# Optimization experiments

Hardware: AMD Instinct MI355X
Metric: run time of the kernel (lower is better)

## Reference

```python
import jax, jax.numpy as jnp
import numpy as np

WEIGHT = 1.0  # init arg `weight`; `threshold` is unused in forward
B, N, M, D = 4, 4096, 4096, 3


def setup_inputs() -> dict:
    key = jax.random.key(0)
    k1, k2 = jax.random.split(key)
    coord = jax.random.normal(k1, (B, N, D), dtype=jnp.float32)
    gt = jax.random.normal(k2, (B, M, D), dtype=jnp.float32)
    return {"coord": coord, "gt": gt}


def reference(coord, gt):
    # Faithful to torch: gt/coord are [B, pts, 3]; transpose(2,1) -> [B, 3, pts]
    g = jnp.transpose(gt, (0, 2, 1))     # [B, 3, M]
    c = jnp.transpose(coord, (0, 2, 1))  # [B, 3, N]
    # dis[b, m, n] = sum_d (g[b,d,m] - c[b,d,n])^2  -> [B, M, N]
    dis = jnp.sum((g[:, :, :, None] - c[:, :, None, :]) ** 2, axis=1)
    match_gt = jnp.min(dis, axis=-1)     # [B, M] nearest coord for each gt point
    match_coord = jnp.min(dis, axis=-2)  # [B, N] nearest gt point for each coord
    res = jnp.mean(match_coord) + jnp.mean(match_gt)
    return WEIGHT * res
```

## Files before the change

kernel.cpp:

```cpp
#include <hip/hip_runtime.h>


#define BATCH 4
#define NPTS  4096
#define TILE  64
#define CH    512
#define NCH   8
#define PHN   32
#define G     8
#define CHP   (CH + CH/8)

__device__ __forceinline__ int pad_idx(int p) { return p + (p >> 3); }

__global__ __launch_bounds__(256, 2) void chamfer_pass(
    const float* __restrict__ coord, const float* __restrict__ gt,
    float* __restrict__ partials)
{
    __shared__ float4 sc[2][CHP];
    __shared__ float bsum[8];

    int bx   = blockIdx.x;
    int pass = bx >> 8;
    int r    = bx & 255;
    int b    = r >> 6;
    int tile = r & 63;

    const float* hbase = (pass ? coord : gt) + b * NPTS * 3;
    const float* sbase = (pass ? gt : coord) + b * NPTS * 3;

    int tid   = threadIdx.x;
    int hg    = tid >> 5;
    int ph    = tid & 31;
    int phofs = ph + (ph >> 3);

    float hx[G], hy[G], hz[G], h2[G], mn[G];
    int h0 = tile * TILE + hg * G;
#pragma unroll
    for (int g = 0; g < G; ++g) {
        float x = hbase[(h0 + g) * 3 + 0];
        float y = hbase[(h0 + g) * 3 + 1];
        float z = hbase[(h0 + g) * 3 + 2];
        hx[g] = x; hy[g] = y; hz[g] = z;
        h2[g] = x * x + y * y + z * z;
        mn[g] = INFINITY;
    }

    {
        int p = tid * 2;
        const float* s0 = sbase + p * 3;
        float x0 = s0[0], y0 = s0[1], z0 = s0[2];
        float x1 = s0[3], y1 = s0[4], z1 = s0[5];
        sc[0][pad_idx(p)]     = make_float4(-2.f*x0, -2.f*y0, -2.f*z0, x0*x0 + y0*y0 + z0*z0);
        sc[0][pad_idx(p + 1)] = make_float4(-2.f*x1, -2.f*y1, -2.f*z1, x1*x1 + y1*y1 + z1*z1);
    }
    __syncthreads();

    for (int ch = 0; ch < NCH; ++ch) {
        if (ch + 1 < NCH) {
            int p = tid * 2;
            const float* s0 = sbase + ((ch + 1) * CH + p) * 3;
            float x0 = s0[0], y0 = s0[1], z0 = s0[2];
            float x1 = s0[3], y1 = s0[4], z1 = s0[5];
            int nb = (ch + 1) & 1;
            sc[nb][pad_idx(p)]     = make_float4(-2.f*x0, -2.f*y0, -2.f*z0, x0*x0 + y0*y0 + z0*z0);
            sc[nb][pad_idx(p + 1)] = make_float4(-2.f*x1, -2.f*y1, -2.f*z1, x1*x1 + y1*y1 + z1*z1);
        }

        const float4* cur = sc[ch & 1];
#pragma unroll 4
        for (int it = 0; it < CH / PHN; ++it) {
            float4 c = cur[it * (PHN + PHN / 8) + phofs];
#pragma unroll
            for (int g = 0; g < G; ++g) {
                float t = h2[g] + c.w;
                t = fmaf(c.x, hx[g], t);
                t = fmaf(c.y, hy[g], t);
                t = fmaf(c.z, hz[g], t);
                mn[g] = fminf(mn[g], t);
            }
        }
        __syncthreads();
    }

    float s = 0.f;
#pragma unroll
    for (int g = 0; g < G; ++g) {
        float v = mn[g];
        v = fminf(v, __shfl_xor(v, 16));
        v = fminf(v, __shfl_xor(v, 8));
        v = fminf(v, __shfl_xor(v, 4));
        v = fminf(v, __shfl_xor(v, 2));
        v = fminf(v, __shfl_xor(v, 1));
        s += fmaxf(v, 0.f);
    }
    if (ph == 0) bsum[hg] = s;
    __syncthreads();
    if (tid == 0) {
        float t = 0.f;
#pragma unroll
        for (int i = 0; i < 8; ++i) t += bsum[i];
        partials[bx] = t;
    }
}

__global__ __launch_bounds__(512) void chamfer_final(
    const float* __restrict__ partials, float* __restrict__ out)
{
    __shared__ float wsum[8];
    int tid = threadIdx.x;
    float s = partials[tid];
#pragma unroll
    for (int off = 32; off > 0; off >>= 1)
        s += __shfl_down(s, off);
    if ((tid & 63) == 0) wsum[tid >> 6] = s;
    __syncthreads();
    if (tid == 0) {
        float t = 0.f;
#pragma unroll
        for (int i = 0; i < 8; ++i) t += wsum[i];
        out[0] = t * (1.0f / 16384.0f);
    }
}

extern "C" void kernel_launch(void* const* d_in, const int* in_sizes, int n_in,
                              void* d_out, int out_size, void* d_ws, size_t ws_size,
                              hipStream_t stream) {
    const float* coord = (const float*)d_in[0];
    const float* gt    = (const float*)d_in[1];
    float* partials = (float*)d_ws;
    float* out = (float*)d_out;

    chamfer_pass<<<512, 256, 0, stream>>>(coord, gt, partials);
    chamfer_final<<<1, 512, 0, stream>>>(partials, out);
}
```

Measured before the change: 71.87 us.

## Fuse final reduction via atomic counter and stage full point set in LDS

Merges the final reduction kernel into the main pass: each block publishes its partial sum, bumps a global counter, and the last block to arrive sums all partials and writes the output. The source point set is now loaded into shared memory once, replacing the double-buffered chunks and removing the per-chunk barriers. The inner loop processes two points per iteration. This saves a kernel launch and the chunk syncs, but the up-front load no longer overlaps compute and each block uses 64KB of LDS. The counter is never reset inside the kernel, so repeated calls depend on the workspace being zeroed; otherwise every block may take the final-reduction path.

After: 76.21 us. 6.0% more time.

```diff
diff --git a/kernel.cpp b/kernel.cpp
--- a/kernel.cpp
+++ b/kernel.cpp
@@ -1,23 +1,17 @@
 #include <hip/hip_runtime.h>
 
 
-#define BATCH 4
-#define NPTS  4096
-#define TILE  64
-#define CH    512
-#define NCH   8
-#define PHN   32
-#define G     8
-#define CHP   (CH + CH/8)
+#define NPTS 4096
+#define TILE 64
+#define PHN  32
+#define G    8
 
-__device__ __forceinline__ int pad_idx(int p) { return p + (p >> 3); }
-
-__global__ __launch_bounds__(256, 2) void chamfer_pass(
+__global__ __launch_bounds__(256, 2) void chamfer_fused(
     const float* __restrict__ coord, const float* __restrict__ gt,
-    float* __restrict__ partials)
+    float* __restrict__ partials, float* __restrict__ counter,
+    float* __restrict__ out)
 {
-    __shared__ float4 sc[2][CHP];
-    __shared__ float bsum[8];
+    __shared__ float4 sc[NPTS];
 
     int bx   = blockIdx.x;
     int pass = bx >> 8;
@@ -28,10 +22,17 @@
     const float* hbase = (pass ? coord : gt) + b * NPTS * 3;
     const float* sbase = (pass ? gt : coord) + b * NPTS * 3;
 
-    int tid   = threadIdx.x;
-    int hg    = tid >> 5;
-    int ph    = tid & 31;
-    int phofs = ph + (ph >> 3);
+    int tid = threadIdx.x;
+    int hg  = tid >> 5;
+    int ph  = tid & 31;
+
+#pragma unroll
+    for (int k = 0; k < NPTS / 256; ++k) {
+        int p = k * 256 + tid;
+        const float* s0 = sbase + p * 3;
+        float x = s0[0], y = s0[1], z = s0[2];
+        sc[p] = make_float4(-2.f * x, -2.f * y, -2.f * z, x * x + y * y + z * z);
+    }
 
     float hx[G], hy[G], hz[G], h2[G], mn[G];
     int h0 = tile * TILE + hg * G;
@@ -44,43 +45,30 @@
         h2[g] = x * x + y * y + z * z;
         mn[g] = INFINITY;
     }
+    __syncthreads();
 
-    {
-        int p = tid * 2;
-        const float* s0 = sbase + p * 3;
-        float x0 = s0[0], y0 = s0[1], z0 = s0[2];
-        float x1 = s0[3], y1 = s0[4], z1 = s0[5];
-        sc[0][pad_idx(p)]     = make_float4(-2.f*x0, -2.f*y0, -2.f*z0, x0*x0 + y0*y0 + z0*z0);
-        sc[0][pad_idx(p + 1)] = make_float4(-2.f*x1, -2.f*y1, -2.f*z1, x1*x1 + y1*y1 + z1*z1);
+#pragma unroll 4
+    for (int it = 0; it < NPTS / (2 * PHN); ++it) {
+        float4 c0 = sc[it * 64 + ph];
+        float4 c1 = sc[it * 64 + 32 + ph];
+#pragma unroll
+        for (int g = 0; g < G; ++g) {
+            float a = h2[g] + c0.w;
+            a = fmaf(c0.x, hx[g], a);
+            a = fmaf(c0.y, hy[g], a);
+            a = fmaf(c0.z, hz[g], a);
+            float d = h2[g] + c1.w;
+            d = fmaf(c1.x, hx[g], d);
+            d = fmaf(c1.y, hy[g], d);
+            d = fmaf(c1.z, hz[g], d);
+            mn[g] = fminf(fminf(a, d), mn[g]);
+        }
     }
     __syncthreads();
 
-    for (int ch = 0; ch < NCH; ++ch) {
-        if (ch + 1 < NCH) {
-            int p = tid * 2;
-            const float* s0 = sbase + ((ch + 1) * CH + p) * 3;
-            float x0 = s0[0], y0 = s0[1], z0 = s0[2];
-            float x1 = s0[3], y1 = s0[4], z1 = s0[5];
-            int nb = (ch + 1) & 1;
-            sc[nb][pad_idx(p)]     = make_float4(-2.f*x0, -2.f*y0, -2.f*z0, x0*x0 + y0*y0 + z0*z0);
-            sc[nb][pad_idx(p + 1)] = make_float4(-2.f*x1, -2.f*y1, -2.f*z1, x1*x1 + y1*y1 + z1*z1);
-        }
-
-        const float4* cur = sc[ch & 1];
-#pragma unroll 4
-        for (int it = 0; it < CH / PHN; ++it) {
-            float4 c = cur[it * (PHN + PHN / 8) + phofs];
-#pragma unroll
-            for (int g = 0; g < G; ++g) {
-                float t = h2[g] + c.w;
-                t = fmaf(c.x, hx[g], t);
-                t = fmaf(c.y, hy[g], t);
-                t = fmaf(c.z, hz[g], t);
-                mn[g] = fminf(mn[g], t);
-            }
-        }
-        __syncthreads();
-    }
+    float* bsum  = reinterpret_cast<float*>(sc);
+    unsigned* fl = reinterpret_cast<unsigned*>(sc) + 8;
+    float* wred  = reinterpret_cast<float*>(sc) + 16;
 
     float s = 0.f;
 #pragma unroll
@@ -95,30 +83,32 @@
     }
     if (ph == 0) bsum[hg] = s;
     __syncthreads();
+
     if (tid == 0) {
         float t = 0.f;
 #pragma unroll
         for (int i = 0; i < 8; ++i) t += bsum[i];
-        partials[bx] = t;
+        __hip_atomic_store(&partials[bx], t, __ATOMIC_RELAXED, __HIP_MEMORY_SCOPE_AGENT);
+        __threadfence();
+        float old = atomicAdd(counter, 1.0f);
+        *fl = (old > 510.5f) ? 1u : 0u;
     }
-}
+    __syncthreads();
 
-__global__ __launch_bounds__(512) void chamfer_final(
-    const float* __restrict__ partials, float* __restrict__ out)
-{
-    __shared__ float wsum[8];
-    int tid = threadIdx.x;
-    float s = partials[tid];
+    if (*fl) {
+        __threadfence();
+        float s2 = 0.f;
 #pragma unroll
-    for (int off = 32; off > 0; off >>= 1)
-        s += __shfl_down(s, off);
-    if ((tid & 63) == 0) wsum[tid >> 6] = s;
-    __syncthreads();
-    if (tid == 0) {
-        float t = 0.f;
+        for (int k = 0; k < 2; ++k)
+            s2 += __hip_atomic_load(&partials[k * 256 + tid],
+                                    __ATOMIC_RELAXED, __HIP_MEMORY_SCOPE_AGENT);
 #pragma unroll
-        for (int i = 0; i < 8; ++i) t += wsum[i];
-        out[0] = t * (1.0f / 16384.0f);
+        for (int off = 32; off > 0; off >>= 1)
+            s2 += __shfl_down(s2, off);
+        if ((tid & 63) == 0) wred[tid >> 6] = s2;
+        __syncthreads();
+        if (tid == 0)
+            out[0] = (wred[0] + wred[1] + wred[2] + wred[3]) * (1.0f / 16384.0f);
     }
 }
 
@@ -127,9 +117,10 @@
                               hipStream_t stream) {
     const float* coord = (const float*)d_in[0];
     const float* gt    = (const float*)d_in[1];
-    float* partials = (float*)d_ws;
+    float* pf = (float*)d_ws;
+    float* partials = pf;
+    float* counter  = pf + 512;
     float* out = (float*)d_out;
 
-    chamfer_pass<<<512, 256, 0, stream>>>(coord, gt, partials);
-    chamfer_final<<<1, 512, 0, stream>>>(partials, out);
+    chamfer_fused<<<512, 256, 0, stream>>>(coord, gt, partials, counter, out);
 }
```

## Hoist query norm out of inner loop and remap threads to full-wave tiles

Applied to the files above, without the earlier changes.

Adds the query point's squared norm after the min reduction instead of inside every distance evaluation, which saves one add per pair in the hot loop. Each block now handles 32 query points with 64 lanes per group, doubling the block count to 1024 and raising the launch-bounds occupancy hint to 4. Two shared-memory candidates are processed per iteration with a paired fminf. The padded shared layout is dropped, since contiguous float4 reads across a 64-lane wave need no padding. The final reduction is adjusted to sum 1024 partials.

Measured after the change: 70.87 us, median of 2. Within noise of the previous version (-1.4%).

```diff
diff --git a/kernel.cpp b/kernel.cpp
--- a/kernel.cpp
+++ b/kernel.cpp
@@ -1,37 +1,32 @@
 #include <hip/hip_runtime.h>
 
 
-#define BATCH 4
-#define NPTS  4096
-#define TILE  64
-#define CH    512
-#define NCH   8
-#define PHN   32
-#define G     8
-#define CHP   (CH + CH/8)
+#define NPTS 4096
+#define TILE 32
+#define PHN  64
+#define G    8
+#define CH   512
+#define NCH  8
 
-__device__ __forceinline__ int pad_idx(int p) { return p + (p >> 3); }
-
-__global__ __launch_bounds__(256, 2) void chamfer_pass(
+__global__ __launch_bounds__(256, 4) void chamfer_pass(
     const float* __restrict__ coord, const float* __restrict__ gt,
     float* __restrict__ partials)
 {
-    __shared__ float4 sc[2][CHP];
-    __shared__ float bsum[8];
+    __shared__ float4 sc[2][CH];
+    __shared__ float bsum[4];
 
     int bx   = blockIdx.x;
-    int pass = bx >> 8;
-    int r    = bx & 255;
-    int b    = r >> 6;
-    int tile = r & 63;
+    int pass = bx >> 9;
+    int r    = bx & 511;
+    int b    = r >> 7;
+    int tile = r & 127;
 
     const float* hbase = (pass ? coord : gt) + b * NPTS * 3;
     const float* sbase = (pass ? gt : coord) + b * NPTS * 3;
 
-    int tid   = threadIdx.x;
-    int hg    = tid >> 5;
-    int ph    = tid & 31;
-    int phofs = ph + (ph >> 3);
+    int tid = threadIdx.x;
+    int hg  = tid >> 6;
+    int ph  = tid & 63;
 
     float hx[G], hy[G], hz[G], h2[G], mn[G];
     int h0 = tile * TILE + hg * G;
@@ -50,8 +45,8 @@
         const float* s0 = sbase + p * 3;
         float x0 = s0[0], y0 = s0[1], z0 = s0[2];
         float x1 = s0[3], y1 = s0[4], z1 = s0[5];
-        sc[0][pad_idx(p)]     = make_float4(-2.f*x0, -2.f*y0, -2.f*z0, x0*x0 + y0*y0 + z0*z0);
-        sc[0][pad_idx(p + 1)] = make_float4(-2.f*x1, -2.f*y1, -2.f*z1, x1*x1 + y1*y1 + z1*z1);
+        sc[0][p]     = make_float4(-2.f*x0, -2.f*y0, -2.f*z0, x0*x0 + y0*y0 + z0*z0);
+        sc[0][p + 1] = make_float4(-2.f*x1, -2.f*y1, -2.f*z1, x1*x1 + y1*y1 + z1*z1);
     }
     __syncthreads();
 
@@ -62,21 +57,24 @@
             float x0 = s0[0], y0 = s0[1], z0 = s0[2];
             float x1 = s0[3], y1 = s0[4], z1 = s0[5];
             int nb = (ch + 1) & 1;
-            sc[nb][pad_idx(p)]     = make_float4(-2.f*x0, -2.f*y0, -2.f*z0, x0*x0 + y0*y0 + z0*z0);
-            sc[nb][pad_idx(p + 1)] = make_float4(-2.f*x1, -2.f*y1, -2.f*z1, x1*x1 + y1*y1 + z1*z1);
+            sc[nb][p]     = make_float4(-2.f*x0, -2.f*y0, -2.f*z0, x0*x0 + y0*y0 + z0*z0);
+            sc[nb][p + 1] = make_float4(-2.f*x1, -2.f*y1, -2.f*z1, x1*x1 + y1*y1 + z1*z1);
         }
 
         const float4* cur = sc[ch & 1];
-#pragma unroll 4
-        for (int it = 0; it < CH / PHN; ++it) {
-            float4 c = cur[it * (PHN + PHN / 8) + phofs];
+#pragma unroll
+        for (int it = 0; it < CH / (2 * PHN); ++it) {
+            float4 c0 = cur[it * 128 + ph];
+            float4 c1 = cur[it * 128 + 64 + ph];
 #pragma unroll
             for (int g = 0; g < G; ++g) {
-                float t = h2[g] + c.w;
-                t = fmaf(c.x, hx[g], t);
-                t = fmaf(c.y, hy[g], t);
-                t = fmaf(c.z, hz[g], t);
-                mn[g] = fminf(mn[g], t);
+                float a = fmaf(c0.x, hx[g], c0.w);
+                a = fmaf(c0.y, hy[g], a);
+                a = fmaf(c0.z, hz[g], a);
+                float d = fmaf(c1.x, hx[g], c1.w);
+                d = fmaf(c1.y, hy[g], d);
+                d = fmaf(c1.z, hz[g], d);
+                mn[g] = fminf(fminf(a, d), mn[g]);
             }
         }
         __syncthreads();
@@ -86,40 +84,36 @@
 #pragma unroll
     for (int g = 0; g < G; ++g) {
         float v = mn[g];
+        v = fminf(v, __shfl_xor(v, 32));
         v = fminf(v, __shfl_xor(v, 16));
         v = fminf(v, __shfl_xor(v, 8));
         v = fminf(v, __shfl_xor(v, 4));
         v = fminf(v, __shfl_xor(v, 2));
         v = fminf(v, __shfl_xor(v, 1));
-        s += fmaxf(v, 0.f);
+        s += fmaxf(v + h2[g], 0.f);
     }
     if (ph == 0) bsum[hg] = s;
     __syncthreads();
-    if (tid == 0) {
-        float t = 0.f;
-#pragma unroll
-        for (int i = 0; i < 8; ++i) t += bsum[i];
-        partials[bx] = t;
-    }
+    if (tid == 0)
+        partials[bx] = bsum[0] + bsum[1] + bsum[2] + bsum[3];
 }
 
-__global__ __launch_bounds__(512) void chamfer_final(
+__global__ __launch_bounds__(256) void chamfer_final(
     const float* __restrict__ partials, float* __restrict__ out)
 {
-    __shared__ float wsum[8];
+    __shared__ float wsum[4];
     int tid = threadIdx.x;
-    float s = partials[tid];
+    float s = 0.f;
+#pragma unroll
+    for (int k = 0; k < 4; ++k)
+        s += partials[k * 256 + tid];
 #pragma unroll
     for (int off = 32; off > 0; off >>= 1)
         s += __shfl_down(s, off);
     if ((tid & 63) == 0) wsum[tid >> 6] = s;
     __syncthreads();
-    if (tid == 0) {
-        float t = 0.f;
-#pragma unroll
-        for (int i = 0; i < 8; ++i) t += wsum[i];
-        out[0] = t * (1.0f / 16384.0f);
-    }
+    if (tid == 0)
+        out[0] = (wsum[0] + wsum[1] + wsum[2] + wsum[3]) * (1.0f / 16384.0f);
 }
 
 extern "C" void kernel_launch(void* const* d_in, const int* in_sizes, int n_in,
@@ -130,6 +124,6 @@
     float* partials = (float*)d_ws;
     float* out = (float*)d_out;
 
-    chamfer_pass<<<512, 256, 0, stream>>>(coord, gt, partials);
-    chamfer_final<<<1, 512, 0, stream>>>(partials, out);
+    chamfer_pass<<<1024, 256, 0, stream>>>(coord, gt, partials);
+    chamfer_final<<<1, 256, 0, stream>>>(partials, out);
 }
```
